# Kernel tuning notes

Measured on AMD Instinct MI355X. Metric: run time of the kernel, lower is better.

Reference implementation:

```python
import jax, jax.numpy as jnp
import numpy as np
from jax import lax

NUM_C_TYPES = 6
TTYPE_UNKNOWN = 5
E = 6            # num_experts_C
D = 1024         # embed_dim
H = D // 4       # gate hidden
TOP_K = 1
TEMP = 0.1
FLOOR = min(0.05, 0.15 / 4)   # routing_floor property (num_experts_B = 4)
CAP_LOW, CAP_HIGH, T_MAX = 0.5, 0.6, 1000


def _build_base_assignment():
    base = np.zeros((NUM_C_TYPES, E), dtype=np.float32)
    for t_type in range(NUM_C_TYPES - 1):
        base[t_type, t_type % E] = 1.0
    base[TTYPE_UNKNOWN] = 1.0 / E
    num_known = NUM_C_TYPES - 1
    if E > num_known:
        for extra_idx in range(num_known, E):
            base[extra_idx % num_known, extra_idx] = 0.3
        for t_type in range(NUM_C_TYPES - 1):
            s = base[t_type].sum()
            if s > 0:
                base[t_type] /= s
    return jnp.asarray(base)


def setup_inputs() -> dict:
    key = jax.random.key(0)
    k1, k2, k3, k4, k5 = jax.random.split(key, 5)
    B, N = 8, 4096
    tokens = jax.random.normal(k1, (B, N, D), dtype=jnp.float32)
    token_types = jax.random.randint(k2, (B, N), 0, NUM_C_TYPES, dtype=jnp.int64)
    t = jax.random.randint(k3, (B,), 0, T_MAX, dtype=jnp.int64)
    # second_gate params; xavier_uniform with gain=0.01
    lim1 = 0.01 * np.sqrt(6.0 / (D + H))
    lim2 = 0.01 * np.sqrt(6.0 / (H + E))
    W1 = jax.random.uniform(k4, (D, H), minval=-lim1, maxval=lim1, dtype=jnp.float32)
    b1 = jnp.zeros((H,), dtype=jnp.float32)
    W2 = jax.random.uniform(k5, (H, E), minval=-lim2, maxval=lim2, dtype=jnp.float32)
    b2 = jnp.zeros((E,), dtype=jnp.float32)
    return {"tokens": tokens, "token_types": token_types, "t": t,
            "W1": W1, "b1": b1, "W2": W2, "b2": b2,
            "base_assignment": _build_base_assignment()}


def _hard_cap(probs, t):
    # TokenLevelHardCap.apply (note faithful cap formula: low + (high + low) * t_norm)
    t_norm = t.astype(probs.dtype) / T_MAX
    cap = (CAP_LOW + (CAP_HIGH + CAP_LOW) * t_norm)[:, None, None]  # (B,1,1)
    excess = jax.nn.relu(probs - cap)
    capped = probs - excess
    headroom = jax.nn.relu(cap - capped)
    headroom_sum = jnp.clip(headroom.sum(-1, keepdims=True), 1e-8, None)
    capped = capped + excess.sum(-1, keepdims=True) * (headroom / headroom_sum)
    return capped


def reference(tokens, token_types, t, W1, b1, W2, b2, base_assignment):
    B, N, _ = tokens.shape
    # primary: deterministic type -> expert assignment (gather)
    base_probs = base_assignment[token_types]                 # (B,N,E)
    # secondary: 2-layer MLP gate, temperature-scaled logits
    h = jax.nn.gelu(jnp.einsum('bnd,dh->bnh', tokens, W1) + b1, approximate=False)
    secondary_logits = (jnp.einsum('bnh,he->bne', h, W2) + b2) / TEMP
    is_unknown = (token_types == TTYPE_UNKNOWN)[..., None].astype(tokens.dtype)
    # faithful to source: unknown tokens blend in raw logits (not softmax probs)
    probs = (1.0 - is_unknown) * base_probs + is_unknown * secondary_logits
    # routing floor interpolation toward uniform
    alpha = min(FLOOR * E, 1.0)
    probs = (1.0 - alpha) * probs + alpha * (1.0 / E)
    # top-k scatter mask
    vals, idx = lax.top_k(probs, TOP_K)                       # (B,N,k)
    dispatch = (jax.nn.one_hot(idx, E, dtype=probs.dtype) * vals[..., None]).sum(-2)
    # no_grad hard cap with redistribution
    dispatch = lax.stop_gradient(_hard_cap(dispatch, t))
    combine = dispatch / (dispatch.sum(-1, keepdims=True) + 1e-8)
    return dispatch, combine
```

## Files before the change

kernel.cpp:

```cpp
#include <hip/hip_runtime.h>
#include <math.h>

#define NUM_E 6
#define DIM 1024
#define HID 256
#define NTOK 32768
#define NPB 4096
#define TTYPE_UNKNOWN 5
#define ONE_MINUS_ALPHA 0.775f
#define FLOOR_TERM 0.0375f
#define GRP 8
#define KSPLIT 8
#define KSPAN 128
#define CPT 4

__device__ __forceinline__ void finalize_and_write(const float probs[NUM_E], float cap,
                                                   float* __restrict__ disp_out,
                                                   float* __restrict__ comb_out) {
    float v = probs[0];
    int bi = 0;
#pragma unroll
    for (int e = 1; e < NUM_E; ++e) {
        if (probs[e] > v) { v = probs[e]; bi = e; }
    }
    float excess = fmaxf(v - cap, 0.0f);
    float capped = v - excess;
    float hr_idx = fmaxf(cap - capped, 0.0f);
    float hsum = fmaxf(hr_idx + 5.0f * cap, 1e-8f);
    float disp[NUM_E];
    float other = excess * cap / hsum;
#pragma unroll
    for (int e = 0; e < NUM_E; ++e) disp[e] = other;
    disp[bi] = capped + excess * hr_idx / hsum;
    float s = 0.0f;
#pragma unroll
    for (int e = 0; e < NUM_E; ++e) s += disp[e];
    float inv = 1.0f / (s + 1e-8f);
#pragma unroll
    for (int e = 0; e < NUM_E; ++e) {
        disp_out[e] = disp[e];
        comb_out[e] = disp[e] * inv;
    }
}

__launch_bounds__(256)
__global__ void classify_kernel(const int* __restrict__ ttypes,
                                const int* __restrict__ tarr,
                                const float* __restrict__ base,
                                float* __restrict__ out,
                                int* __restrict__ cnt,
                                int* __restrict__ list) {
    int i = blockIdx.x * blockDim.x + threadIdx.x;
    if (i >= NTOK) return;
    int ty = ttypes[i];
    if (ty == TTYPE_UNKNOWN) {
        int pos = atomicAdd(cnt, 1);
        list[pos] = i;
        return;
    }
    int b = i / NPB;
    float tnorm = (float)tarr[b] / 1000.0f;
    float cap = 0.5f + 1.1f * tnorm;
    float probs[NUM_E];
#pragma unroll
    for (int e = 0; e < NUM_E; ++e)
        probs[e] = ONE_MINUS_ALPHA * base[ty * NUM_E + e] + FLOOR_TERM;
    finalize_and_write(probs, cap,
                       out + (size_t)i * NUM_E,
                       out + (size_t)NTOK * NUM_E + (size_t)i * NUM_E);
}

__launch_bounds__(512)
__global__ void mlp_kernel(const float* __restrict__ tokens,
                           const int* __restrict__ tarr,
                           const float* __restrict__ W1,
                           const float* __restrict__ b1,
                           const float* __restrict__ W2,
                           const float* __restrict__ b2,
                           float* __restrict__ out,
                           const int* __restrict__ cnt,
                           const int* __restrict__ list) {
    __shared__ float smem[GRP * DIM];
    __shared__ float w2s[HID * NUM_E];
    __shared__ float ls[GRP][NUM_E];

    int count = cnt[0];
    int start = blockIdx.x * GRP;
    if (start >= count) return;
    int tid = threadIdx.x;

    float (*xs)[DIM] = (float (*)[DIM])smem;

    {
        int slot = tid & 255;
        int rr = tid >> 8;
#pragma unroll
        for (int p = 0; p < 4; ++p) {
            int r = rr * 4 + p;
            int idx = start + r;
            if (idx > count - 1) idx = count - 1;
            int tok = list[idx];
            const float4* src = reinterpret_cast<const float4*>(tokens + (size_t)tok * DIM);
            reinterpret_cast<float4*>(xs[r])[slot] = src[slot];
        }
    }
    for (int kk = tid; kk < HID * NUM_E; kk += 512) w2s[kk] = W2[kk];
    __syncthreads();

    int cg = tid & 63;
    int ks = tid >> 6;
    int kbase = ks * KSPAN;

    float acc[GRP][CPT];
#pragma unroll
    for (int r = 0; r < GRP; ++r)
#pragma unroll
        for (int c = 0; c < CPT; ++c) acc[r][c] = 0.0f;

    const float* w1p = W1 + (size_t)kbase * HID + cg;
    const float* xb[GRP];
#pragma unroll
    for (int r = 0; r < GRP; ++r) xb[r] = &xs[r][kbase];

#pragma unroll 1
    for (int k = 0; k < KSPAN; k += 4) {
        float w[4][CPT];
        const float* wp = w1p + (size_t)k * HID;
#pragma unroll
        for (int kk = 0; kk < 4; ++kk)
#pragma unroll
            for (int c = 0; c < CPT; ++c)
                w[kk][c] = wp[kk * HID + 64 * c];
#pragma unroll
        for (int r = 0; r < GRP; ++r) {
            float4 xq = *reinterpret_cast<const float4*>(xb[r] + k);
#pragma unroll
            for (int c = 0; c < CPT; ++c) {
                acc[r][c] = fmaf(xq.x, w[0][c], acc[r][c]);
                acc[r][c] = fmaf(xq.y, w[1][c], acc[r][c]);
                acc[r][c] = fmaf(xq.z, w[2][c], acc[r][c]);
                acc[r][c] = fmaf(xq.w, w[3][c], acc[r][c]);
            }
        }
    }
    __syncthreads();

    float (*hp)[HID] = (float (*)[HID])smem;
    float (*hs)[HID + 1] = (float (*)[HID + 1])(smem + 2048);

    const float kc = 0.70710678118654752f;
#pragma unroll 1
    for (int r = 0; r < GRP; ++r) {
#pragma unroll
        for (int c = 0; c < CPT; ++c) hp[ks][cg + 64 * c] = acc[r][c];
        __syncthreads();
        if (tid < HID) {
            float s = hp[0][tid];
#pragma unroll
            for (int q = 1; q < KSPLIT; ++q) s += hp[q][tid];
            float pre = s + b1[tid];
            hs[r][tid] = 0.5f * pre * (1.0f + erff(pre * kc));
        }
        __syncthreads();
    }

    if (tid < GRP * NUM_E) {
        int r = tid / NUM_E, e = tid % NUM_E;
        float s = 0.0f;
        for (int j = 0; j < HID; ++j) s = fmaf(hs[r][j], w2s[j * NUM_E + e], s);
        ls[r][e] = (s + b2[e]) / 0.1f;
    }
    __syncthreads();

    if (tid < GRP && start + tid < count) {
        int tokidx = list[start + tid];
        int b = tokidx / NPB;
        float tnorm = (float)tarr[b] / 1000.0f;
        float cap = 0.5f + 1.1f * tnorm;
        float probs[NUM_E];
#pragma unroll
        for (int e = 0; e < NUM_E; ++e)
            probs[e] = ONE_MINUS_ALPHA * ls[tid][e] + FLOOR_TERM;
        finalize_and_write(probs, cap,
                           out + (size_t)tokidx * NUM_E,
                           out + (size_t)NTOK * NUM_E + (size_t)tokidx * NUM_E);
    }
}

extern "C" void kernel_launch(void* const* d_in, const int* in_sizes, int n_in,
                              void* d_out, int out_size, void* d_ws, size_t ws_size,
                              hipStream_t stream) {
    const float* tokens = (const float*)d_in[0];
    const int*   ttypes = (const int*)d_in[1];
    const int*   tarr   = (const int*)d_in[2];
    const float* W1     = (const float*)d_in[3];
    const float* b1     = (const float*)d_in[4];
    const float* W2     = (const float*)d_in[5];
    const float* b2     = (const float*)d_in[6];
    const float* base   = (const float*)d_in[7];
    float* out = (float*)d_out;

    int* cnt  = (int*)d_ws;
    int* list = (int*)d_ws + 64;

    hipMemsetAsync(cnt, 0, sizeof(int), stream);
    classify_kernel<<<NTOK / 256, 256, 0, stream>>>(ttypes, tarr, base, out, cnt, list);
    mlp_kernel<<<NTOK / GRP, 512, 0, stream>>>(tokens, tarr, W1, b1, W2, b2,
                                               out, cnt, list);
}
```

Baseline: 69.94 us.

## Retile MLP first layer to 8 contiguous columns per thread with float4 W1 loads

Each thread now owns 8 contiguous hidden columns over a 64-wide K slice (16 K-splits), instead of 4 strided columns over a 128-wide slice, so W1 can be read with float4 vector loads. This raises register-level reuse of each x value from 4 to 8 FMAs and cuts load instruction count. The partial-sum reduction buffer doubles to 16 rows, and the launch bounds now request more blocks per CU. The tradeoffs are a 64-float accumulator per thread, which adds register pressure, and LDS bank conflicts when each thread writes 8 contiguous values.

```diff
diff --git a/kernel.cpp b/kernel.cpp
--- a/kernel.cpp
+++ b/kernel.cpp
@@ -10,9 +10,9 @@
 #define ONE_MINUS_ALPHA 0.775f
 #define FLOOR_TERM 0.0375f
 #define GRP 8
-#define KSPLIT 8
-#define KSPAN 128
-#define CPT 4
+#define KSPLIT 16
+#define KSPAN 64
+#define CPT 8
 
 __device__ __forceinline__ void finalize_and_write(const float probs[NUM_E], float cap,
                                                    float* __restrict__ disp_out,
@@ -70,16 +70,16 @@
                        out + (size_t)NTOK * NUM_E + (size_t)i * NUM_E);
 }
 
-__launch_bounds__(512)
-__global__ void mlp_kernel(const float* __restrict__ tokens,
-                           const int* __restrict__ tarr,
-                           const float* __restrict__ W1,
-                           const float* __restrict__ b1,
-                           const float* __restrict__ W2,
-                           const float* __restrict__ b2,
-                           float* __restrict__ out,
-                           const int* __restrict__ cnt,
-                           const int* __restrict__ list) {
+__global__ __launch_bounds__(512, 4)
+void mlp_kernel(const float* __restrict__ tokens,
+                const int* __restrict__ tarr,
+                const float* __restrict__ W1,
+                const float* __restrict__ b1,
+                const float* __restrict__ W2,
+                const float* __restrict__ b2,
+                float* __restrict__ out,
+                const int* __restrict__ cnt,
+                const int* __restrict__ list) {
     __shared__ float smem[GRP * DIM];
     __shared__ float w2s[HID * NUM_E];
     __shared__ float ls[GRP][NUM_E];
@@ -107,9 +107,10 @@
     for (int kk = tid; kk < HID * NUM_E; kk += 512) w2s[kk] = W2[kk];
     __syncthreads();
 
-    int cg = tid & 63;
-    int ks = tid >> 6;
+    int cg = tid & 31;
+    int ks = tid >> 5;
     int kbase = ks * KSPAN;
+    int colbase = cg * CPT;
 
     float acc[GRP][CPT];
 #pragma unroll
@@ -117,42 +118,67 @@
 #pragma unroll
         for (int c = 0; c < CPT; ++c) acc[r][c] = 0.0f;
 
-    const float* w1p = W1 + (size_t)kbase * HID + cg;
+    const float* w1p = W1 + (size_t)kbase * HID + colbase;
     const float* xb[GRP];
 #pragma unroll
     for (int r = 0; r < GRP; ++r) xb[r] = &xs[r][kbase];
 
 #pragma unroll 1
     for (int k = 0; k < KSPAN; k += 4) {
-        float w[4][CPT];
+        float4 wa[4], wb[4];
         const float* wp = w1p + (size_t)k * HID;
 #pragma unroll
-        for (int kk = 0; kk < 4; ++kk)
-#pragma unroll
-            for (int c = 0; c < CPT; ++c)
-                w[kk][c] = wp[kk * HID + 64 * c];
+        for (int kk = 0; kk < 4; ++kk) {
+            wa[kk] = *reinterpret_cast<const float4*>(wp + kk * HID);
+            wb[kk] = *reinterpret_cast<const float4*>(wp + kk * HID + 4);
+        }
 #pragma unroll
         for (int r = 0; r < GRP; ++r) {
             float4 xq = *reinterpret_cast<const float4*>(xb[r] + k);
-#pragma unroll
-            for (int c = 0; c < CPT; ++c) {
-                acc[r][c] = fmaf(xq.x, w[0][c], acc[r][c]);
-                acc[r][c] = fmaf(xq.y, w[1][c], acc[r][c]);
-                acc[r][c] = fmaf(xq.z, w[2][c], acc[r][c]);
-                acc[r][c] = fmaf(xq.w, w[3][c], acc[r][c]);
-            }
+            acc[r][0] = fmaf(xq.x, wa[0].x, acc[r][0]);
+            acc[r][1] = fmaf(xq.x, wa[0].y, acc[r][1]);
+            acc[r][2] = fmaf(xq.x, wa[0].z, acc[r][2]);
+            acc[r][3] = fmaf(xq.x, wa[0].w, acc[r][3]);
+            acc[r][4] = fmaf(xq.x, wb[0].x, acc[r][4]);
+            acc[r][5] = fmaf(xq.x, wb[0].y, acc[r][5]);
+            acc[r][6] = fmaf(xq.x, wb[0].z, acc[r][6]);
+            acc[r][7] = fmaf(xq.x, wb[0].w, acc[r][7]);
+            acc[r][0] = fmaf(xq.y, wa[1].x, acc[r][0]);
+            acc[r][1] = fmaf(xq.y, wa[1].y, acc[r][1]);
+            acc[r][2] = fmaf(xq.y, wa[1].z, acc[r][2]);
+            acc[r][3] = fmaf(xq.y, wa[1].w, acc[r][3]);
+            acc[r][4] = fmaf(xq.y, wb[1].x, acc[r][4]);
+            acc[r][5] = fmaf(xq.y, wb[1].y, acc[r][5]);
+            acc[r][6] = fmaf(xq.y, wb[1].z, acc[r][6]);
+            acc[r][7] = fmaf(xq.y, wb[1].w, acc[r][7]);
+            acc[r][0] = fmaf(xq.z, wa[2].x, acc[r][0]);
+            acc[r][1] = fmaf(xq.z, wa[2].y, acc[r][1]);
+            acc[r][2] = fmaf(xq.z, wa[2].z, acc[r][2]);
+            acc[r][3] = fmaf(xq.z, wa[2].w, acc[r][3]);
+            acc[r][4] = fmaf(xq.z, wb[2].x, acc[r][4]);
+            acc[r][5] = fmaf(xq.z, wb[2].y, acc[r][5]);
+            acc[r][6] = fmaf(xq.z, wb[2].z, acc[r][6]);
+            acc[r][7] = fmaf(xq.z, wb[2].w, acc[r][7]);
+            acc[r][0] = fmaf(xq.w, wa[3].x, acc[r][0]);
+            acc[r][1] = fmaf(xq.w, wa[3].y, acc[r][1]);
+            acc[r][2] = fmaf(xq.w, wa[3].z, acc[r][2]);
+            acc[r][3] = fmaf(xq.w, wa[3].w, acc[r][3]);
+            acc[r][4] = fmaf(xq.w, wb[3].x, acc[r][4]);
+            acc[r][5] = fmaf(xq.w, wb[3].y, acc[r][5]);
+            acc[r][6] = fmaf(xq.w, wb[3].z, acc[r][6]);
+            acc[r][7] = fmaf(xq.w, wb[3].w, acc[r][7]);
         }
     }
     __syncthreads();
 
     float (*hp)[HID] = (float (*)[HID])smem;
-    float (*hs)[HID + 1] = (float (*)[HID + 1])(smem + 2048);
+    float (*hs)[HID + 1] = (float (*)[HID + 1])(smem + 4096);
 
     const float kc = 0.70710678118654752f;
 #pragma unroll 1
     for (int r = 0; r < GRP; ++r) {
 #pragma unroll
-        for (int c = 0; c < CPT; ++c) hp[ks][cg + 64 * c] = acc[r][c];
+        for (int c = 0; c < CPT; ++c) hp[ks][colbase + c] = acc[r][c];
         __syncthreads();
         if (tid < HID) {
             float s = hp[0][tid];
```

Measured after the change: 127.1 us. 81.7% more time.
